# Performance work log

Hardware: AMD Instinct MI355X
Metric: run time of the kernel (lower is better)

## Reference

```python
import jax, jax.numpy as jnp
import numpy as np

B, S, D, H = 4, 2048, 1024, 16
HD = D // H  # head dim = 64
EPS = 1e-12


def setup_inputs() -> dict:
    key = jax.random.key(0)
    ks = jax.random.split(key, 9)
    sc = 1.0 / np.sqrt(D)
    return {
        "X": jax.random.normal(ks[0], (B, S, D), jnp.float32),
        "Wq": jax.random.normal(ks[1], (D, D), jnp.float32) * sc,
        "bq": jnp.zeros((D,), jnp.float32),
        "Wk": jax.random.normal(ks[2], (D, D), jnp.float32) * sc,
        "bk": jnp.zeros((D,), jnp.float32),
        "Wv": jax.random.normal(ks[3], (D, D), jnp.float32) * sc,
        "bv": jnp.zeros((D,), jnp.float32),
        "Wo": jax.random.normal(ks[4], (D, D), jnp.float32) * sc,
        "bo": jnp.zeros((D,), jnp.float32),
        "gamma": jnp.ones((D,), jnp.float32),
        "beta": jnp.zeros((D,), jnp.float32),
    }


def _attention_block(X, Wq, bq, Wk, bk, Wv, bv, Wo, bo, gamma, beta):
    def heads(t):  # [B,S,D] -> [B,H,S,HD]
        return t.reshape(B, S, H, HD).transpose(0, 2, 1, 3)

    Q = heads(X @ Wq.T + bq)
    K = heads(X @ Wk.T + bk)
    V = heads(X @ Wv.T + bv)
    A = jnp.einsum("bhqd,bhkd->bhqk", Q, K) / np.sqrt(HD)
    A = jax.nn.softmax(A, axis=-1)
    O = jnp.einsum("bhqk,bhkd->bhqd", A, V)
    O = O.transpose(0, 2, 1, 3).reshape(B, S, D)
    O = O @ Wo.T + bo
    Y = O + X
    mu = Y.mean(-1, keepdims=True)
    var = jnp.square(Y - mu).mean(-1, keepdims=True)
    return gamma * (Y - mu) / jnp.sqrt(var + EPS) + beta


def reference(X, Wq, bq, Wk, bk, Wv, bv, Wo, bo, gamma, beta):
    return _attention_block(X, Wq, bq, Wk, bk, Wv, bv, Wo, bo, gamma, beta)
```

## Files before the change

kernel.cpp:

```cpp
#include <hip/hip_runtime.h>
#include <hip/hip_bf16.h>

#define B_ 4
#define S_ 2048
#define D_ 1024
#define H_ 16
#define HD_ 64
#define M_ (B_*S_)
#define BH_ (B_*H_)

typedef __bf16 bf16;
typedef __attribute__((ext_vector_type(8))) __bf16 bf16x8;
typedef __attribute__((ext_vector_type(4))) __bf16 bf16x4;
typedef __attribute__((ext_vector_type(4))) float f32x4;
typedef __attribute__((ext_vector_type(16))) float f32x16;
typedef __attribute__((ext_vector_type(4))) unsigned u32x4;

#define MFMA16(a,b,c) __builtin_amdgcn_mfma_f32_16x16x32_bf16((a),(b),(c),0,0,0)
#define MFMA32(a,b,c) __builtin_amdgcn_mfma_f32_32x32x16_bf16((a),(b),(c),0,0,0)

__device__ __forceinline__ void gl2lds16(const void* g, void* l) {
  __builtin_amdgcn_global_load_lds(
      (__attribute__((address_space(1))) void*)(g),
      (__attribute__((address_space(3))) void*)(l), 16, 0, 0);
}

__device__ __forceinline__ float fexp2(float x) {
  float r;
  asm("v_exp_f32 %0, %1" : "=v"(r) : "v"(x));
  return r;
}

__device__ __forceinline__ unsigned cvtpk(float lo, float hi) {
  unsigned r;
  asm("v_cvt_pk_bf16_f32 %0, %1, %2" : "=v"(r) : "v"(lo), "v"(hi));
  return r;
}

__global__ __launch_bounds__(256) void k_cvt(const float* __restrict__ in,
                                             bf16* __restrict__ out, int n) {
  int i = (blockIdx.x * 256 + threadIdx.x) * 4;
  if (i >= n) return;
  f32x4 v = *(const f32x4*)(in + i);
  bf16x4 o;
  o[0] = (bf16)v[0]; o[1] = (bf16)v[1]; o[2] = (bf16)v[2]; o[3] = (bf16)v[3];
  *(bf16x4*)(out + i) = o;
}

template <int EPI>
__global__ __launch_bounds__(512, 4) void k_gemm(const bf16* __restrict__ A,
                                                 const bf16* __restrict__ W,
                                                 const float* __restrict__ bias,
                                                 const float* __restrict__ Xres,
                                                 void* __restrict__ outp,
                                                 float scale) {
  __shared__ __align__(16) bf16 As[2][128 * 64];
  __shared__ __align__(16) bf16 Bs[2][128 * 64];
  const int t = threadIdx.x;
  const int l = t & 63, w = t >> 6;
  const int g = l >> 4, c = l & 15;
  const int wm = w >> 2, wn = w & 3;
  const int m0 = blockIdx.y * 128, n0 = blockIdx.x * 128;

  f32x4 acc[4][2];
#pragma unroll
  for (int i = 0; i < 4; ++i)
#pragma unroll
    for (int j = 0; j < 2; ++j) acc[i][j] = (f32x4)(0.0f);

  const int srow = t >> 3;
  const int schk = t & 7;

#define STG(buf, k0)                                                          \
  do {                                                                        \
    for (int p = 0; p < 2; ++p) {                                             \
      const int row = p * 64 + srow;                                          \
      const int sc = (schk ^ (row & 7)) * 8;                                  \
      gl2lds16(A + (size_t)(m0 + row) * D_ + (k0) + sc,                       \
               &As[buf][p * 4096 + t * 8]);                                   \
      gl2lds16(W + (size_t)(n0 + row) * D_ + (k0) + sc,                       \
               &Bs[buf][p * 4096 + t * 8]);                                   \
    }                                                                         \
  } while (0)

  STG(0, 0);
  __syncthreads();

  for (int kt = 0; kt < D_ / 64; ++kt) {
    const int cur = kt & 1;
    if (kt + 1 < D_ / 64) STG(cur ^ 1, (kt + 1) * 64);
#pragma unroll
    for (int kk = 0; kk < 2; ++kk) {
      bf16x8 af[4], bw[2];
#pragma unroll
      for (int i = 0; i < 4; ++i) {
        const int ra = wm * 64 + i * 16 + c;
        af[i] = *(const bf16x8*)&As[cur][ra * 64 + (((kk * 4 + g) ^ (ra & 7)) * 8)];
      }
#pragma unroll
      for (int j = 0; j < 2; ++j) {
        const int rb = wn * 32 + j * 16 + c;
        bw[j] = *(const bf16x8*)&Bs[cur][rb * 64 + (((kk * 4 + g) ^ (rb & 7)) * 8)];
      }
#pragma unroll
      for (int i = 0; i < 4; ++i)
#pragma unroll
        for (int j = 0; j < 2; ++j) acc[i][j] = MFMA16(af[i], bw[j], acc[i][j]);
    }
    __syncthreads();
  }
#undef STG

  float bv[2];
#pragma unroll
  for (int j = 0; j < 2; ++j) bv[j] = bias[n0 + wn * 32 + j * 16 + c];

#pragma unroll
  for (int i = 0; i < 4; ++i) {
#pragma unroll
    for (int j = 0; j < 2; ++j) {
#pragma unroll
      for (int r = 0; r < 4; ++r) {
        const int m = m0 + wm * 64 + i * 16 + g * 4 + r;
        const int n = n0 + wn * 32 + j * 16 + c;
        const float v = (acc[i][j][r] + bv[j]) * scale;
        if (EPI == 2) {
          ((float*)outp)[(size_t)m * D_ + n] = v + Xres[(size_t)m * D_ + n];
        } else {
          const int b = m >> 11, s = m & (S_ - 1);
          const int h = n >> 6, hd = n & 63;
          size_t idx;
          if (EPI == 0) idx = (((size_t)(b * H_ + h)) * S_ + s) * HD_ + hd;
          else          idx = (((size_t)(b * H_ + h)) * HD_ + hd) * S_ + s;
          ((bf16*)outp)[idx] = (bf16)v;
        }
      }
    }
  }
}

__global__ __launch_bounds__(256, 3) void k_attn(const bf16* __restrict__ Q,
                                                 const bf16* __restrict__ K,
                                                 const bf16* __restrict__ Vt,
                                                 bf16* __restrict__ O) {
  __shared__ __align__(16) bf16 Ks[2][64 * 64];
  __shared__ __align__(16) bf16 Vs[2][64 * 64];
  const int t = threadIdx.x;
  const int l = t & 63, w = t >> 6;
  const int c32 = l & 31, hi = l >> 5;
  const int bh = blockIdx.y;
  const int q0 = blockIdx.x * 128 + w * 32;
  const bf16* Qh = Q + (size_t)bh * S_ * HD_;
  const bf16* Kh = K + (size_t)bh * S_ * HD_;
  const bf16* Vh = Vt + (size_t)bh * HD_ * S_;

  bf16x8 qf[4];
#pragma unroll
  for (int kk = 0; kk < 4; ++kk)
    qf[kk] = *(const bf16x8*)&Qh[(size_t)(q0 + c32) * HD_ + kk * 16 + hi * 8];

  f32x16 acc0 = (f32x16)(0.f), acc1 = (f32x16)(0.f);
  float m_c = -__builtin_inff(), l_c = 0.f;

  const int srow = t >> 3, schk = t & 7;
  const int sw = c32 & 7;

#define STGA(buf, kt)                                                         \
  do {                                                                        \
    for (int p = 0; p < 2; ++p) {                                             \
      const int row = p * 32 + srow;                                          \
      const int sc = (schk ^ (row & 7)) * 8;                                  \
      gl2lds16(Kh + (size_t)((kt) * 64 + row) * HD_ + sc,                     \
               &Ks[buf][p * 2048 + t * 8]);                                   \
      gl2lds16(Vh + (size_t)row * S_ + (kt) * 64 + sc,                        \
               &Vs[buf][p * 2048 + t * 8]);                                   \
    }                                                                         \
  } while (0)

  STGA(0, 0);
  __syncthreads();

  for (int kt = 0; kt < S_ / 64; ++kt) {
    const int cur = kt & 1;
    if (kt + 1 < S_ / 64) STGA(cur ^ 1, kt + 1);

    f32x16 st0 = (f32x16)(0.f), st1 = (f32x16)(0.f);
    __builtin_amdgcn_s_setprio(1);
#pragma unroll
    for (int kk = 0; kk < 4; ++kk) {
      const int slot = ((kk * 2 + hi) ^ sw) * 8;
      bf16x8 kf0 = *(const bf16x8*)&Ks[cur][c32 * 64 + slot];
      bf16x8 kf1 = *(const bf16x8*)&Ks[cur][(32 + c32) * 64 + slot];
      st0 = MFMA32(kf0, qf[kk], st0);
      st1 = MFMA32(kf1, qf[kk], st1);
    }
    __builtin_amdgcn_s_setprio(0);

    float tm;
    {
      f32x16 mx;
#pragma unroll
      for (int r = 0; r < 16; ++r) mx[r] = fmaxf(st0[r], st1[r]);
      float m8[8];
#pragma unroll
      for (int r = 0; r < 8; ++r) m8[r] = fmaxf(mx[r], mx[r + 8]);
      float m4[4];
#pragma unroll
      for (int r = 0; r < 4; ++r) m4[r] = fmaxf(m8[r], m8[r + 4]);
      tm = fmaxf(fmaxf(m4[0], m4[1]), fmaxf(m4[2], m4[3]));
      tm = fmaxf(tm, __shfl_xor(tm, 32));
    }
    if (!__all(tm <= m_c + 8.f)) {
      const float mn = fmaxf(m_c, tm);
      const float cf = fexp2(m_c - mn);
      m_c = mn;
      l_c *= cf;
#pragma unroll
      for (int r = 0; r < 16; ++r) { acc0[r] *= cf; acc1[r] *= cf; }
    }
    float rs = 0.f;
#pragma unroll
    for (int r = 0; r < 16; ++r) { st0[r] = fexp2(st0[r] - m_c); rs += st0[r]; }
#pragma unroll
    for (int r = 0; r < 16; ++r) { st1[r] = fexp2(st1[r] - m_c); rs += st1[r]; }
    rs += __shfl_xor(rs, 32);
    l_c += rs;

    unsigned ca[8], cb[8];
#pragma unroll
    for (int i = 0; i < 8; ++i) {
      ca[i] = cvtpk(st0[2 * i], st0[2 * i + 1]);
      cb[i] = cvtpk(st1[2 * i], st1[2 * i + 1]);
    }
    asm volatile("v_permlane32_swap_b32 %0, %1" : "+v"(ca[0]), "+v"(ca[2]));
    asm volatile("v_permlane32_swap_b32 %0, %1" : "+v"(ca[1]), "+v"(ca[3]));
    asm volatile("v_permlane32_swap_b32 %0, %1" : "+v"(ca[4]), "+v"(ca[6]));
    asm volatile("v_permlane32_swap_b32 %0, %1" : "+v"(ca[5]), "+v"(ca[7]));
    asm volatile("v_permlane32_swap_b32 %0, %1" : "+v"(cb[0]), "+v"(cb[2]));
    asm volatile("v_permlane32_swap_b32 %0, %1" : "+v"(cb[1]), "+v"(cb[3]));
    asm volatile("v_permlane32_swap_b32 %0, %1" : "+v"(cb[4]), "+v"(cb[6]));
    asm volatile("v_permlane32_swap_b32 %0, %1" : "+v"(cb[5]), "+v"(cb[7]));
    bf16x8 pf[4];
    pf[0] = __builtin_bit_cast(bf16x8, (u32x4){ca[0], ca[1], ca[2], ca[3]});
    pf[1] = __builtin_bit_cast(bf16x8, (u32x4){ca[4], ca[5], ca[6], ca[7]});
    pf[2] = __builtin_bit_cast(bf16x8, (u32x4){cb[0], cb[1], cb[2], cb[3]});
    pf[3] = __builtin_bit_cast(bf16x8, (u32x4){cb[4], cb[5], cb[6], cb[7]});

    __builtin_amdgcn_s_setprio(1);
#pragma unroll
    for (int kb = 0; kb < 4; ++kb) {
      const int slot = ((kb * 2 + hi) ^ sw) * 8;
      bf16x8 vf0 = *(const bf16x8*)&Vs[cur][c32 * 64 + slot];
      bf16x8 vf1 = *(const bf16x8*)&Vs[cur][(32 + c32) * 64 + slot];
      acc0 = MFMA32(vf0, pf[kb], acc0);
      acc1 = MFMA32(vf1, pf[kb], acc1);
    }
    __builtin_amdgcn_s_setprio(0);

    __syncthreads();
  }
#undef STGA

  const float li = 1.f / l_c;
  const int b = bh >> 4, h = bh & 15;
  const int q = q0 + c32;
  bf16* Orow = O + ((size_t)(b * S_ + q)) * D_ + h * 64;
#pragma unroll
  for (int rq = 0; rq < 4; ++rq) {
    bf16x4 o0, o1;
#pragma unroll
    for (int j = 0; j < 4; ++j) {
      o0[j] = (bf16)(acc0[rq * 4 + j] * li);
      o1[j] = (bf16)(acc1[rq * 4 + j] * li);
    }
    *(bf16x4*)&Orow[rq * 8 + hi * 4] = o0;
    *(bf16x4*)&Orow[32 + rq * 8 + hi * 4] = o1;
  }
}

__global__ __launch_bounds__(256) void k_ln(const float* __restrict__ Y,
                                            const float* __restrict__ gamma,
                                            const float* __restrict__ beta,
                                            float* __restrict__ out) {
  __shared__ float red[8];
  const int row = blockIdx.x, t = threadIdx.x;
  const float* y = Y + (size_t)row * D_;
  f32x4 v = *(const f32x4*)(y + t * 4);
  float s = v[0] + v[1] + v[2] + v[3];
  float s2 = v[0]*v[0] + v[1]*v[1] + v[2]*v[2] + v[3]*v[3];
#pragma unroll
  for (int mk = 1; mk <= 32; mk <<= 1) {
    s += __shfl_xor(s, mk);
    s2 += __shfl_xor(s2, mk);
  }
  if ((t & 63) == 0) { red[t >> 6] = s; red[4 + (t >> 6)] = s2; }
  __syncthreads();
  const float ts = red[0] + red[1] + red[2] + red[3];
  const float ts2 = red[4] + red[5] + red[6] + red[7];
  const float mu = ts * (1.0f / D_);
  const float inv = rsqrtf(ts2 * (1.0f / D_) - mu * mu + 1e-12f);
  f32x4 gm = *(const f32x4*)(gamma + t * 4);
  f32x4 bt = *(const f32x4*)(beta + t * 4);
  f32x4 o;
#pragma unroll
  for (int j = 0; j < 4; ++j) o[j] = gm[j] * (v[j] - mu) * inv + bt[j];
  *(f32x4*)(out + (size_t)row * D_ + t * 4) = o;
}

extern "C" void kernel_launch(void* const* d_in, const int* in_sizes, int n_in,
                              void* d_out, int out_size, void* d_ws, size_t ws_size,
                              hipStream_t stream) {
  const float* X     = (const float*)d_in[0];
  const float* Wq    = (const float*)d_in[1];
  const float* bq    = (const float*)d_in[2];
  const float* Wk    = (const float*)d_in[3];
  const float* bk    = (const float*)d_in[4];
  const float* Wv    = (const float*)d_in[5];
  const float* bv    = (const float*)d_in[6];
  const float* Wo    = (const float*)d_in[7];
  const float* bo    = (const float*)d_in[8];
  const float* gamma = (const float*)d_in[9];
  const float* beta  = (const float*)d_in[10];

  char* ws = (char*)d_ws;
  bf16* Xb  = (bf16*)(ws + 0);
  bf16* Wqb = (bf16*)(ws + (16u << 20));
  bf16* Wkb = (bf16*)(ws + (18u << 20));
  bf16* Wvb = (bf16*)(ws + (20u << 20));
  bf16* Wob = (bf16*)(ws + (22u << 20));
  bf16* Qb  = (bf16*)(ws + (24u << 20));
  bf16* Kb  = (bf16*)(ws + (40u << 20));
  bf16* Vt  = (bf16*)(ws + (56u << 20));
  bf16* Ob  = (bf16*)(ws + (72u << 20));
  float* Yb = (float*)(ws + (88u << 20));

  const float SCL = 0.125f * 1.44269504088896340736f;

  k_cvt<<<M_ * D_ / 1024, 256, 0, stream>>>(X, Xb, M_ * D_);
  k_cvt<<<D_ * D_ / 1024, 256, 0, stream>>>(Wq, Wqb, D_ * D_);
  k_cvt<<<D_ * D_ / 1024, 256, 0, stream>>>(Wk, Wkb, D_ * D_);
  k_cvt<<<D_ * D_ / 1024, 256, 0, stream>>>(Wv, Wvb, D_ * D_);
  k_cvt<<<D_ * D_ / 1024, 256, 0, stream>>>(Wo, Wob, D_ * D_);

  dim3 gg(D_ / 128, M_ / 128);
  k_gemm<0><<<gg, 512, 0, stream>>>(Xb, Wqb, bq, nullptr, Qb, SCL);
  k_gemm<0><<<gg, 512, 0, stream>>>(Xb, Wkb, bk, nullptr, Kb, 1.0f);
  k_gemm<1><<<gg, 512, 0, stream>>>(Xb, Wvb, bv, nullptr, Vt, 1.0f);
  k_attn<<<dim3(S_ / 128, BH_), 256, 0, stream>>>(Qb, Kb, Vt, Ob);
  k_gemm<2><<<gg, 512, 0, stream>>>(Ob, Wob, bo, X, Yb, 1.0f);
  k_ln<<<M_, 256, 0, stream>>>(Yb, gamma, beta, (float*)d_out);
}
```

Measured before the change: 329.9 us.

## Fuse QKV GEMMs, use fragment-ordered LDS layout, remap blocks across XCDs

The three Q/K/V projection GEMMs become one launch over a concatenated weight matrix, and each output section picks its own bias, scale and layout in the epilogue. Both GEMMs and the attention kernel stage LDS tiles in MFMA-fragment order, so every lane reads a contiguous 16-byte chunk with no XOR swizzle. Block indices are remapped so consecutive logical tiles are spread round-robin over the 8 XCDs for better L2 locality. Attention occupancy is raised from 3 to 4 blocks per CU. The fragment layout may add bank conflicts on the global-to-LDS writes, and the higher occupancy target may cause register spills.

```diff
diff --git a/kernel.cpp b/kernel.cpp
--- a/kernel.cpp
+++ b/kernel.cpp
@@ -47,39 +47,41 @@
   *(bf16x4*)(out + i) = o;
 }
 
-template <int EPI>
-__global__ __launch_bounds__(512, 4) void k_gemm(const bf16* __restrict__ A,
-                                                 const bf16* __restrict__ W,
-                                                 const float* __restrict__ bias,
-                                                 const float* __restrict__ Xres,
-                                                 void* __restrict__ outp,
-                                                 float scale) {
-  __shared__ __align__(16) bf16 As[2][128 * 64];
-  __shared__ __align__(16) bf16 Bs[2][128 * 64];
+__global__ __launch_bounds__(512, 4) void k_gemm_qkv(
+    const bf16* __restrict__ A, const bf16* __restrict__ Wc,
+    const float* __restrict__ bq, const float* __restrict__ bk,
+    const float* __restrict__ bvp,
+    bf16* __restrict__ Qb, bf16* __restrict__ Kb, bf16* __restrict__ Vt,
+    float scl_q) {
+  __shared__ __align__(16) bf16 As[2][16 * 512];
+  __shared__ __align__(16) bf16 Bs[2][16 * 512];
   const int t = threadIdx.x;
   const int l = t & 63, w = t >> 6;
   const int g = l >> 4, c = l & 15;
   const int wm = w >> 2, wn = w & 3;
-  const int m0 = blockIdx.y * 128, n0 = blockIdx.x * 128;
+
+  const int bid = blockIdx.x;
+  const int lg = (bid & 7) * 192 + (bid >> 3);
+  const int xt = lg % 24, yt = lg / 24;
+  const int m0 = yt * 128, n0 = xt * 128;
+  const int sec = n0 >> 10;
 
   f32x4 acc[4][2];
 #pragma unroll
   for (int i = 0; i < 4; ++i)
 #pragma unroll
     for (int j = 0; j < 2; ++j) acc[i][j] = (f32x4)(0.0f);
-
-  const int srow = t >> 3;
-  const int schk = t & 7;
 
 #define STG(buf, k0)                                                          \
   do {                                                                        \
     for (int p = 0; p < 2; ++p) {                                             \
-      const int row = p * 64 + srow;                                          \
-      const int sc = (schk ^ (row & 7)) * 8;                                  \
-      gl2lds16(A + (size_t)(m0 + row) * D_ + (k0) + sc,                       \
-               &As[buf][p * 4096 + t * 8]);                                   \
-      gl2lds16(W + (size_t)(n0 + row) * D_ + (k0) + sc,                       \
-               &Bs[buf][p * 4096 + t * 8]);                                   \
+      const int f = p * 8 + w;                                                \
+      const int row = (f >> 1) * 16 + (l & 15);                               \
+      const int kc = (f & 1) * 4 + (l >> 4);                                  \
+      gl2lds16(A + (size_t)(m0 + row) * D_ + (k0) + kc * 8,                   \
+               &As[buf][f * 512]);                                            \
+      gl2lds16(Wc + (size_t)(n0 + row) * D_ + (k0) + kc * 8,                  \
+               &Bs[buf][f * 512]);                                            \
     }                                                                         \
   } while (0)
 
@@ -93,17 +95,101 @@
     for (int kk = 0; kk < 2; ++kk) {
       bf16x8 af[4], bw[2];
 #pragma unroll
-      for (int i = 0; i < 4; ++i) {
-        const int ra = wm * 64 + i * 16 + c;
-        af[i] = *(const bf16x8*)&As[cur][ra * 64 + (((kk * 4 + g) ^ (ra & 7)) * 8)];
+      for (int i = 0; i < 4; ++i)
+        af[i] = *(const bf16x8*)&As[cur][(((wm * 4 + i) * 2 + kk) * 512) + l * 8];
+#pragma unroll
+      for (int j = 0; j < 2; ++j)
+        bw[j] = *(const bf16x8*)&Bs[cur][(((wn * 2 + j) * 2 + kk) * 512) + l * 8];
+#pragma unroll
+      for (int i = 0; i < 4; ++i)
+#pragma unroll
+        for (int j = 0; j < 2; ++j) acc[i][j] = MFMA16(af[i], bw[j], acc[i][j]);
+    }
+    __syncthreads();
+  }
+#undef STG
+
+  const float* bptr = (sec == 0) ? bq : (sec == 1) ? bk : bvp;
+  const float scl = (sec == 0) ? scl_q : 1.0f;
+  bf16* outp = (sec == 0) ? Qb : (sec == 1) ? Kb : Vt;
+  const int nbase = (n0 & 1023) + wn * 32;
+
+  float bvj[2];
+#pragma unroll
+  for (int j = 0; j < 2; ++j) bvj[j] = bptr[nbase + j * 16 + c];
+
+#pragma unroll
+  for (int i = 0; i < 4; ++i) {
+#pragma unroll
+    for (int j = 0; j < 2; ++j) {
+#pragma unroll
+      for (int r = 0; r < 4; ++r) {
+        const int m = m0 + wm * 64 + i * 16 + g * 4 + r;
+        const int nloc = nbase + j * 16 + c;
+        const float v = (acc[i][j][r] + bvj[j]) * scl;
+        const int b = m >> 11, s = m & (S_ - 1);
+        const int h = nloc >> 6, hd = nloc & 63;
+        size_t idx;
+        if (sec < 2) idx = (((size_t)(b * H_ + h)) * S_ + s) * HD_ + hd;
+        else         idx = (((size_t)(b * H_ + h)) * HD_ + hd) * S_ + s;
+        outp[idx] = (bf16)v;
       }
-#pragma unroll
-      for (int j = 0; j < 2; ++j) {
-        const int rb = wn * 32 + j * 16 + c;
-        bw[j] = *(const bf16x8*)&Bs[cur][rb * 64 + (((kk * 4 + g) ^ (rb & 7)) * 8)];
-      }
+    }
+  }
+}
+
+__global__ __launch_bounds__(512, 4) void k_gemm_o(
+    const bf16* __restrict__ A, const bf16* __restrict__ Wc,
+    const float* __restrict__ bias, const float* __restrict__ Xres,
+    float* __restrict__ Yb) {
+  __shared__ __align__(16) bf16 As[2][16 * 512];
+  __shared__ __align__(16) bf16 Bs[2][16 * 512];
+  const int t = threadIdx.x;
+  const int l = t & 63, w = t >> 6;
+  const int g = l >> 4, c = l & 15;
+  const int wm = w >> 2, wn = w & 3;
+
+  const int bid = blockIdx.x;
+  const int lg = (bid & 7) * 64 + (bid >> 3);
+  const int xt = lg & 7, yt = lg >> 3;
+  const int m0 = yt * 128, n0 = xt * 128;
+
+  f32x4 acc[4][2];
+#pragma unroll
+  for (int i = 0; i < 4; ++i)
+#pragma unroll
+    for (int j = 0; j < 2; ++j) acc[i][j] = (f32x4)(0.0f);
+
+#define STG(buf, k0)                                                          \
+  do {                                                                        \
+    for (int p = 0; p < 2; ++p) {                                             \
+      const int f = p * 8 + w;                                                \
+      const int row = (f >> 1) * 16 + (l & 15);                               \
+      const int kc = (f & 1) * 4 + (l >> 4);                                  \
+      gl2lds16(A + (size_t)(m0 + row) * D_ + (k0) + kc * 8,                   \
+               &As[buf][f * 512]);                                            \
+      gl2lds16(Wc + (size_t)(n0 + row) * D_ + (k0) + kc * 8,                  \
+               &Bs[buf][f * 512]);                                            \
+    }                                                                         \
+  } while (0)
+
+  STG(0, 0);
+  __syncthreads();
+
+  for (int kt = 0; kt < D_ / 64; ++kt) {
+    const int cur = kt & 1;
+    if (kt + 1 < D_ / 64) STG(cur ^ 1, (kt + 1) * 64);
+#pragma unroll
+    for (int kk = 0; kk < 2; ++kk) {
+      bf16x8 af[4], bw[2];
 #pragma unroll
       for (int i = 0; i < 4; ++i)
+        af[i] = *(const bf16x8*)&As[cur][(((wm * 4 + i) * 2 + kk) * 512) + l * 8];
+#pragma unroll
+      for (int j = 0; j < 2; ++j)
+        bw[j] = *(const bf16x8*)&Bs[cur][(((wn * 2 + j) * 2 + kk) * 512) + l * 8];
+#pragma unroll
+      for (int i = 0; i < 4; ++i)
 #pragma unroll
         for (int j = 0; j < 2; ++j) acc[i][j] = MFMA16(af[i], bw[j], acc[i][j]);
     }
@@ -111,9 +197,9 @@
   }
 #undef STG
 
-  float bv[2];
-#pragma unroll
-  for (int j = 0; j < 2; ++j) bv[j] = bias[n0 + wn * 32 + j * 16 + c];
+  float bvj[2];
+#pragma unroll
+  for (int j = 0; j < 2; ++j) bvj[j] = bias[n0 + wn * 32 + j * 16 + c];
 
 #pragma unroll
   for (int i = 0; i < 4; ++i) {
@@ -123,33 +209,28 @@
       for (int r = 0; r < 4; ++r) {
         const int m = m0 + wm * 64 + i * 16 + g * 4 + r;
         const int n = n0 + wn * 32 + j * 16 + c;
-        const float v = (acc[i][j][r] + bv[j]) * scale;
-        if (EPI == 2) {
-          ((float*)outp)[(size_t)m * D_ + n] = v + Xres[(size_t)m * D_ + n];
-        } else {
-          const int b = m >> 11, s = m & (S_ - 1);
-          const int h = n >> 6, hd = n & 63;
-          size_t idx;
-          if (EPI == 0) idx = (((size_t)(b * H_ + h)) * S_ + s) * HD_ + hd;
-          else          idx = (((size_t)(b * H_ + h)) * HD_ + hd) * S_ + s;
-          ((bf16*)outp)[idx] = (bf16)v;
-        }
+        Yb[(size_t)m * D_ + n] =
+            acc[i][j][r] + bvj[j] + Xres[(size_t)m * D_ + n];
       }
     }
   }
 }
 
-__global__ __launch_bounds__(256, 3) void k_attn(const bf16* __restrict__ Q,
+__global__ __launch_bounds__(256, 4) void k_attn(const bf16* __restrict__ Q,
                                                  const bf16* __restrict__ K,
                                                  const bf16* __restrict__ Vt,
                                                  bf16* __restrict__ O) {
-  __shared__ __align__(16) bf16 Ks[2][64 * 64];
-  __shared__ __align__(16) bf16 Vs[2][64 * 64];
+  __shared__ __align__(16) bf16 Ks[2][8 * 512];
+  __shared__ __align__(16) bf16 Vs[2][8 * 512];
   const int t = threadIdx.x;
   const int l = t & 63, w = t >> 6;
   const int c32 = l & 31, hi = l >> 5;
-  const int bh = blockIdx.y;
-  const int q0 = blockIdx.x * 128 + w * 32;
+
+  const int bid = blockIdx.x;
+  const int lg = (bid & 7) * 128 + (bid >> 3);
+  const int bh = lg >> 4;
+  const int q0 = (lg & 15) * 128 + w * 32;
+
   const bf16* Qh = Q + (size_t)bh * S_ * HD_;
   const bf16* Kh = K + (size_t)bh * S_ * HD_;
   const bf16* Vh = Vt + (size_t)bh * HD_ * S_;
@@ -162,18 +243,16 @@
   f32x16 acc0 = (f32x16)(0.f), acc1 = (f32x16)(0.f);
   float m_c = -__builtin_inff(), l_c = 0.f;
 
-  const int srow = t >> 3, schk = t & 7;
-  const int sw = c32 & 7;
-
 #define STGA(buf, kt)                                                         \
   do {                                                                        \
     for (int p = 0; p < 2; ++p) {                                             \
-      const int row = p * 32 + srow;                                          \
-      const int sc = (schk ^ (row & 7)) * 8;                                  \
-      gl2lds16(Kh + (size_t)((kt) * 64 + row) * HD_ + sc,                     \
-               &Ks[buf][p * 2048 + t * 8]);                                   \
-      gl2lds16(Vh + (size_t)row * S_ + (kt) * 64 + sc,                        \
-               &Vs[buf][p * 2048 + t * 8]);                                   \
+      const int f = p * 4 + w;                                                \
+      const int row = (f & 1) * 32 + (l & 31);                                \
+      const int c8 = (f >> 1) * 2 + (l >> 5);                                 \
+      gl2lds16(Kh + (size_t)((kt) * 64 + row) * HD_ + c8 * 8,                 \
+               &Ks[buf][f * 512]);                                            \
+      gl2lds16(Vh + (size_t)row * S_ + (kt) * 64 + c8 * 8,                    \
+               &Vs[buf][f * 512]);                                            \
     }                                                                         \
   } while (0)
 
@@ -188,9 +267,8 @@
     __builtin_amdgcn_s_setprio(1);
 #pragma unroll
     for (int kk = 0; kk < 4; ++kk) {
-      const int slot = ((kk * 2 + hi) ^ sw) * 8;
-      bf16x8 kf0 = *(const bf16x8*)&Ks[cur][c32 * 64 + slot];
-      bf16x8 kf1 = *(const bf16x8*)&Ks[cur][(32 + c32) * 64 + slot];
+      bf16x8 kf0 = *(const bf16x8*)&Ks[cur][(kk * 2) * 512 + l * 8];
+      bf16x8 kf1 = *(const bf16x8*)&Ks[cur][(kk * 2 + 1) * 512 + l * 8];
       st0 = MFMA32(kf0, qf[kk], st0);
       st1 = MFMA32(kf1, qf[kk], st1);
     }
@@ -249,9 +327,8 @@
     __builtin_amdgcn_s_setprio(1);
 #pragma unroll
     for (int kb = 0; kb < 4; ++kb) {
-      const int slot = ((kb * 2 + hi) ^ sw) * 8;
-      bf16x8 vf0 = *(const bf16x8*)&Vs[cur][c32 * 64 + slot];
-      bf16x8 vf1 = *(const bf16x8*)&Vs[cur][(32 + c32) * 64 + slot];
+      bf16x8 vf0 = *(const bf16x8*)&Vs[cur][(kb * 2) * 512 + l * 8];
+      bf16x8 vf1 = *(const bf16x8*)&Vs[cur][(kb * 2 + 1) * 512 + l * 8];
       acc0 = MFMA32(vf0, pf[kb], acc0);
       acc1 = MFMA32(vf1, pf[kb], acc1);
     }
@@ -324,9 +401,7 @@
 
   char* ws = (char*)d_ws;
   bf16* Xb  = (bf16*)(ws + 0);
-  bf16* Wqb = (bf16*)(ws + (16u << 20));
-  bf16* Wkb = (bf16*)(ws + (18u << 20));
-  bf16* Wvb = (bf16*)(ws + (20u << 20));
+  bf16* Wcat= (bf16*)(ws + (16u << 20));
   bf16* Wob = (bf16*)(ws + (22u << 20));
   bf16* Qb  = (bf16*)(ws + (24u << 20));
   bf16* Kb  = (bf16*)(ws + (40u << 20));
@@ -337,16 +412,13 @@
   const float SCL = 0.125f * 1.44269504088896340736f;
 
   k_cvt<<<M_ * D_ / 1024, 256, 0, stream>>>(X, Xb, M_ * D_);
-  k_cvt<<<D_ * D_ / 1024, 256, 0, stream>>>(Wq, Wqb, D_ * D_);
-  k_cvt<<<D_ * D_ / 1024, 256, 0, stream>>>(Wk, Wkb, D_ * D_);
-  k_cvt<<<D_ * D_ / 1024, 256, 0, stream>>>(Wv, Wvb, D_ * D_);
+  k_cvt<<<D_ * D_ / 1024, 256, 0, stream>>>(Wq, Wcat, D_ * D_);
+  k_cvt<<<D_ * D_ / 1024, 256, 0, stream>>>(Wk, Wcat + (size_t)D_ * D_, D_ * D_);
+  k_cvt<<<D_ * D_ / 1024, 256, 0, stream>>>(Wv, Wcat + 2 * (size_t)D_ * D_, D_ * D_);
   k_cvt<<<D_ * D_ / 1024, 256, 0, stream>>>(Wo, Wob, D_ * D_);
 
-  dim3 gg(D_ / 128, M_ / 128);
-  k_gemm<0><<<gg, 512, 0, stream>>>(Xb, Wqb, bq, nullptr, Qb, SCL);
-  k_gemm<0><<<gg, 512, 0, stream>>>(Xb, Wkb, bk, nullptr, Kb, 1.0f);
-  k_gemm<1><<<gg, 512, 0, stream>>>(Xb, Wvb, bv, nullptr, Vt, 1.0f);
-  k_attn<<<dim3(S_ / 128, BH_), 256, 0, stream>>>(Qb, Kb, Vt, Ob);
-  k_gemm<2><<<gg, 512, 0, stream>>>(Ob, Wob, bo, X, Yb, 1.0f);
+  k_gemm_qkv<<<1536, 512, 0, stream>>>(Xb, Wcat, bq, bk, bv, Qb, Kb, Vt, SCL);
+  k_attn<<<1024, 256, 0, stream>>>(Qb, Kb, Vt, Ob);
+  k_gemm_o<<<512, 512, 0, stream>>>(Ob, Wob, bo, X, Yb);
   k_ln<<<M_, 256, 0, stream>>>(Yb, gamma, beta, (float*)d_out);
 }
```

Measured after the change: 382.1 us. 1.16x slower.
